# Optimization experiments

Measured on AMD Instinct MI355X. Metric: run time of the kernel, lower is better.

The kernel has to match this reference:

```python
import jax, jax.numpy as jnp
import numpy as np
from jax import lax

B, HI, WI, D = 8, 64, 64, 128
HO, WO = HI // 2, WI // 2
N_IN, N_OUT = HI * WI, HO * WO
NUM_ITERS = 3
EPS = 1e-6


def _build_indices(Ho, Wo):
    # replicates _build_q_and_in_idx: per coarse position, 9 relative offsets
    dys = np.repeat(np.arange(-1, 2), 3)
    dxs = np.tile(np.arange(-1, 2), 3)
    oy = np.arange(Ho)[:, None, None]
    ox = np.arange(Wo)[None, :, None]
    ny = oy + dys
    nx = ox + dxs
    valid = (ny >= 0) & (ny < Ho) & (nx >= 0) & (nx < Wo)  # (Ho,Wo,9)
    coarse = np.where(valid, ny * Wo + nx, 0)
    base = (oy * Wo + ox) * 9
    g9 = np.where(valid, base + np.arange(9), 0).reshape(-1, 9)
    c9 = coarse.reshape(-1, 9)
    q_idx = np.stack([np.tile(g9, (1, 4))] * 4)
    col_idx = np.stack([np.tile(c9, (1, 4))] * 4)
    in_idx = np.stack([np.tile(np.where(valid, coarse * 4 + h, 0).reshape(-1, 9), (1, 4)) for h in range(4)])
    return q_idx.astype(np.int32), in_idx.astype(np.int32), col_idx.astype(np.int32)


Q_IDX, IN_IDX, COL_IDX = _build_indices(HO, WO)
# NATTEN kernel-3 neighborhoods: window center clamped to stay in-bounds.
NY = np.clip(np.arange(HO) - 1, 0, HO - 3)[:, None] + np.arange(3)  # (HO,3)
NX = np.clip(np.arange(WO) - 1, 0, WO - 3)[:, None] + np.arange(3)  # (WO,3)


def _ln(x, g, b, eps=1e-5):
    mu = x.mean(-1, keepdims=True)
    var = ((x - mu) ** 2).mean(-1, keepdims=True)
    return (x - mu) * lax.rsqrt(var + eps) * g + b


def _forward(x, seed_w, wq, wk, wv, w1, b1, w2, b2, ln_in_g, ln_in_b, ln_out_g, ln_out_b, rpb, tau):
    ny, nx = jnp.asarray(NY), jnp.asarray(NX)
    q_idx = jnp.asarray(Q_IDX)

    def unfold(t):  # (B,HI,WI,D) -> (B,4,HO,WO,D); head = ky*2+kx (F.unfold order)
        return t.reshape(B, HO, 2, WO, 2, D).transpose(0, 2, 4, 1, 3, 5).reshape(B, 4, HO, WO, D)

    k = unfold((_ln(x, ln_in_g, ln_in_b) @ wk.T).reshape(B, HI, WI, D))
    v = unfold((x @ wv.T).reshape(B, HI, WI, D))
    k_n = k[:, :, ny][:, :, :, :, nx]  # (B,4,HO,3,WO,3,D)
    v_n = v[:, :, ny][:, :, :, :, nx]

    x_map = x.reshape(B, HI, WI, D).transpose(0, 3, 1, 2)
    seed = lax.conv_general_dilated(x_map, seed_w, (2, 2), ((1, 1), (1, 1)),
                                    dimension_numbers=('NCHW', 'OIHW', 'NCHW'))
    x_out = _ln(seed.reshape(B, D, N_OUT).transpose(0, 2, 1), ln_out_g, ln_out_b)

    scale = jnp.exp(tau)
    attn36 = a_col_h = None
    for _ in range(NUM_ITERS):
        q = (_ln(x_out, ln_out_g, ln_out_b) @ wq.T).reshape(B, HO, WO, D)
        # na2d_qk (q broadcast over the 4 heads) + relative position bias
        logits = jnp.einsum('byxd,bhykxld->bhyxkl', q, k_n).reshape(B, 4, HO, WO, 9) + rpb.reshape(1, 4, 1, 1, 9)
        attn = jax.nn.softmax(logits * scale, axis=-1) + EPS
        flat = attn.reshape(B, 4, N_OUT * 9)
        attn36 = jnp.take_along_axis(
            flat, jnp.broadcast_to(q_idx.reshape(1, 4, -1), (B, 4, N_OUT * 36)), axis=-1
        ).reshape(B, 4, N_OUT, 36)
        a_col_h = attn36 / (attn36.sum(axis=(1, 3), keepdims=True) + EPS)
        attn9 = a_col_h[..., :9].reshape(B, 4, HO, WO, 3, 3)
        # na2d_av then sum over heads
        updates = jnp.einsum('bhyxkl,bhykxld->byxd', attn9, v_n).reshape(B, N_OUT, D)
        x_out = x_out + updates
        h1 = jax.nn.gelu(x_out @ w1.T + b1, approximate=False)
        x_out = x_out + _ln(h1 @ w2.T + b2, ln_out_g, ln_out_b)
    return x_out, attn36, a_col_h


def setup_inputs() -> dict:
    key = jax.random.key(0)
    ks = jax.random.split(key, 8)
    n = lambda k, shape, s: jax.random.normal(k, shape, jnp.float32) * s
    D2 = 2 * D
    return {
        'x': jax.random.normal(ks[0], (B, N_IN, D), jnp.float32),
        'seed_w': n(ks[1], (D, D, 3, 3), (2.0 / (9 * D)) ** 0.5),
        'wq': n(ks[2], (D, D), D ** -0.5),
        'wk': n(ks[3], (D, D), D ** -0.5),
        'wv': n(ks[4], (D, D), D ** -0.5),
        'w1': n(ks[5], (D2, D), D ** -0.5),
        'b1': jnp.zeros((D2,), jnp.float32),
        'w2': n(ks[6], (D, D2), D2 ** -0.5),
        'b2': jnp.zeros((D,), jnp.float32),
        'ln_in_g': jnp.ones((D,), jnp.float32),
        'ln_in_b': jnp.zeros((D,), jnp.float32),
        'ln_out_g': jnp.ones((D,), jnp.float32),
        'ln_out_b': jnp.zeros((D,), jnp.float32),
        'rpb': n(ks[7], (4, 9), 0.02),
        'tau': jnp.float32(np.log(D ** -0.5)),
    }


def reference(x, seed_w, wq, wk, wv, w1, b1, w2, b2, ln_in_g, ln_in_b, ln_out_g, ln_out_b, rpb, tau):
    x_out, attn36, a_col_h = _forward(x, seed_w, wq, wk, wv, w1, b1, w2, b2,
                                      ln_in_g, ln_in_b, ln_out_g, ln_out_b, rpb, tau)
    # A_col: scatter_add over dim 1 -> A_col[b, in_idx[i,j], j] += a_col_h[b,i,j]
    rows = jnp.asarray(IN_IDX).reshape(4 * N_OUT, 36)
    cols = jnp.broadcast_to(jnp.arange(36), rows.shape)
    A_col = jnp.zeros((B, N_IN, N_OUT), x.dtype).at[:, rows, cols].add(a_col_h.reshape(B, 4 * N_OUT, 36))
    # A_row: scatter_add over dim 2 -> A_row[b, i, col_idx[i,j]] += attn36[b,i,j]
    ri = jnp.broadcast_to(jnp.arange(4 * N_OUT)[:, None], (4 * N_OUT, 36))
    A_row = jnp.zeros((B, N_IN, N_OUT), x.dtype).at[:, ri, jnp.asarray(COL_IDX).reshape(4 * N_OUT, 36)].add(
        attn36.reshape(B, 4 * N_OUT, 36))
    return x_out, A_row, A_col
```

## Files before the change

kernel.cpp:

```cpp
#include <hip/hip_runtime.h>
#include <hip/hip_bf16.h>
#include <math.h>

#define BB   8
#define HI_  64
#define WI_  64
#define DD   128
#define HO_  32
#define WO_  32
#define NIN  4096
#define NOUT 1024
#define LN_EPS 1e-5f
#define ATT_EPS 1e-6f

#define ZSHARE 3932160

typedef short bf16x8 __attribute__((ext_vector_type(8)));
typedef float f32x4  __attribute__((ext_vector_type(4)));

__device__ __forceinline__ ushort f2bf(float f) {
    union { float f; unsigned u; } a; a.f = f;
    unsigned u = a.u;
    return (ushort)((u + 0x7FFFu + ((u >> 16) & 1u)) >> 16);
}
__device__ __forceinline__ float bf2f(ushort u) {
    union { unsigned u; float f; } a; a.u = ((unsigned)u) << 16;
    return a.f;
}

__global__ __launch_bounds__(256)
void wconvert_kernel(const float* __restrict__ wq, const float* __restrict__ wk,
                     const float* __restrict__ wv, const float* __restrict__ w1,
                     const float* __restrict__ w2, const float* __restrict__ sw,
                     ushort* __restrict__ dst)
{
    int i = blockIdx.x * 256 + threadIdx.x;
    float v;
    if (i < 16384)        v = wk[i];
    else if (i < 32768)   v = wv[i - 16384];
    else if (i < 49152) { int j = i - 32768; int d = j >> 7, n = j & 127;
                          v = wq[n * DD + d]; }
    else if (i < 81920)   v = w1[i - 49152];
    else if (i < 114688)  v = w2[i - 81920];
    else {
        int j = i - 114688;
        int n = j / 1152;
        int rem = j - n * 1152;
        int tap = rem >> 7, di = rem & 127;
        v = sw[((size_t)(n * DD + di)) * 9 + tap];
    }
    dst[i] = f2bf(v);
}

__global__ __launch_bounds__(256)
void prep_kernel(const float* __restrict__ x, const ushort* __restrict__ wkb,
                 const ushort* __restrict__ wvb, const ushort* __restrict__ wqTb,
                 const ushort* __restrict__ wcb,
                 const float* __restrict__ ligg, const float* __restrict__ libb,
                 const float* __restrict__ logg, const float* __restrict__ lobb,
                 ushort* __restrict__ k2buf, ushort* __restrict__ vbuf,
                 float* __restrict__ xout, float4* __restrict__ zb)
{
    __shared__ __align__(16) char arena[62208];
    const int tid = threadIdx.x;
    const int wid = tid >> 6, lane = tid & 63;
    const int lr = lane & 15, lk = (lane >> 4) << 3;

    {
        float4* zp = zb + (size_t)blockIdx.x * 6144;
        float4 zz = make_float4(0.f, 0.f, 0.f, 0.f);
        #pragma unroll
        for (int i = 0; i < 24; ++i) zp[i * 256 + tid] = zz;
    }

    if (blockIdx.x < 512) {
        ushort (*Araw)[136] = (ushort (*)[136])(arena);
        ushort (*Aln)[136]  = (ushort (*)[136])(arena + 17408);
        float  (*rstat)[2]  = (float  (*)[2])(arena + 34816);
        const int row0 = blockIdx.x * 64;

        float4 xv[8];
        #pragma unroll
        for (int i = 0; i < 8; ++i) {
            int l = tid + i * 256;
            int r = l >> 5, c4 = (l & 31) << 2;
            float4 v = *(const float4*)(x + (size_t)(row0 + r) * DD + c4);
            xv[i] = v;
            ushort4 o; o.x = f2bf(v.x); o.y = f2bf(v.y); o.z = f2bf(v.z); o.w = f2bf(v.w);
            *(ushort4*)&Araw[r][c4] = o;
            float s  = v.x + v.y + v.z + v.w;
            float s2 = v.x * v.x + v.y * v.y + v.z * v.z + v.w * v.w;
            #pragma unroll
            for (int o2 = 16; o2 > 0; o2 >>= 1) {
                s  += __shfl_down(s,  o2, 32);
                s2 += __shfl_down(s2, o2, 32);
            }
            if ((tid & 31) == 0) {
                float mu = s * (1.f / DD);
                float var = s2 * (1.f / DD) - mu * mu;
                rstat[r][0] = mu; rstat[r][1] = rsqrtf(var + LN_EPS);
            }
        }
        __syncthreads();
        #pragma unroll
        for (int i = 0; i < 8; ++i) {
            int l = tid + i * 256;
            int r = l >> 5, c4 = (l & 31) << 2;
            float mu = rstat[r][0], rs = rstat[r][1];
            float4 v = xv[i];
            ushort4 o;
            o.x = f2bf((v.x - mu) * rs * ligg[c4 + 0] + libb[c4 + 0]);
            o.y = f2bf((v.y - mu) * rs * ligg[c4 + 1] + libb[c4 + 1]);
            o.z = f2bf((v.z - mu) * rs * ligg[c4 + 2] + libb[c4 + 2]);
            o.w = f2bf((v.w - mu) * rs * ligg[c4 + 3] + libb[c4 + 3]);
            *(ushort4*)&Aln[r][c4] = o;
        }
        __syncthreads();

        const int wm = (wid & 1) * 32, wn = (wid >> 1) * 64;
        {
            f32x4 ak[2][4] = {}, av[2][4] = {};
            #pragma unroll
            for (int ks = 0; ks < 4; ++ks) {
                int kk = ks * 32 + lk;
                bf16x8 aL[2], aR[2];
                #pragma unroll
                for (int mi = 0; mi < 2; ++mi) {
                    aL[mi] = *(const bf16x8*)&Aln[wm + mi * 16 + lr][kk];
                    aR[mi] = *(const bf16x8*)&Araw[wm + mi * 16 + lr][kk];
                }
                #pragma unroll
                for (int ni = 0; ni < 4; ++ni) {
                    bf16x8 bK = *(const bf16x8*)(wkb + (size_t)(wn + ni * 16 + lr) * DD + kk);
                    bf16x8 bV = *(const bf16x8*)(wvb + (size_t)(wn + ni * 16 + lr) * DD + kk);
                    #pragma unroll
                    for (int mi = 0; mi < 2; ++mi) {
                        ak[mi][ni] = __builtin_amdgcn_mfma_f32_16x16x32_bf16(aL[mi], bK, ak[mi][ni], 0, 0, 0);
                        av[mi][ni] = __builtin_amdgcn_mfma_f32_16x16x32_bf16(aR[mi], bV, av[mi][ni], 0, 0, 0);
                    }
                }
            }
            #pragma unroll
            for (int mi = 0; mi < 2; ++mi)
                #pragma unroll
                for (int ni = 0; ni < 4; ++ni) {
                    int n = wn + ni * 16 + (lane & 15);
                    #pragma unroll
                    for (int r = 0; r < 4; ++r) {
                        int m = row0 + wm + mi * 16 + ((lane >> 4) << 2) + r;
                        int b = m >> 12, pix = m & 4095;
                        int iy = pix >> 6, ix = pix & 63;
                        int h = ((iy & 1) << 1) | (ix & 1);
                        int cp = ((iy >> 1) << 5) | (ix >> 1);
                        size_t orow = ((size_t)(b * 4 + h) << 10) + cp;
                        vbuf[orow * DD + n] = f2bf(av[mi][ni][r]);
                    }
                }
            __syncthreads();
            #pragma unroll
            for (int mi = 0; mi < 2; ++mi)
                #pragma unroll
                for (int ni = 0; ni < 4; ++ni) {
                    int n = wn + ni * 16 + (lane & 15);
                    #pragma unroll
                    for (int r = 0; r < 4; ++r) {
                        int lm = wm + mi * 16 + ((lane >> 4) << 2) + r;
                        Aln[lm][n] = f2bf(ak[mi][ni][r]);
                    }
                }
        }
        __syncthreads();

        {
            f32x4 a2[2][4] = {};
            #pragma unroll
            for (int ks = 0; ks < 4; ++ks) {
                int kk = ks * 32 + lk;
                bf16x8 aF[2];
                aF[0] = *(const bf16x8*)&Aln[wm + lr][kk];
                aF[1] = *(const bf16x8*)&Aln[wm + 16 + lr][kk];
                #pragma unroll
                for (int ni = 0; ni < 4; ++ni) {
                    bf16x8 bF = *(const bf16x8*)(wqTb + (size_t)(wn + ni * 16 + lr) * DD + kk);
                    a2[0][ni] = __builtin_amdgcn_mfma_f32_16x16x32_bf16(aF[0], bF, a2[0][ni], 0, 0, 0);
                    a2[1][ni] = __builtin_amdgcn_mfma_f32_16x16x32_bf16(aF[1], bF, a2[1][ni], 0, 0, 0);
                }
            }
            #pragma unroll
            for (int mi = 0; mi < 2; ++mi)
                #pragma unroll
                for (int ni = 0; ni < 4; ++ni) {
                    int n = wn + ni * 16 + (lane & 15);
                    #pragma unroll
                    for (int r = 0; r < 4; ++r) {
                        int m = row0 + wm + mi * 16 + ((lane >> 4) << 2) + r;
                        int b = m >> 12, pix = m & 4095;
                        int iy = pix >> 6, ix = pix & 63;
                        int h = ((iy & 1) << 1) | (ix & 1);
                        int cp = ((iy >> 1) << 5) | (ix >> 1);
                        size_t orow = ((size_t)(b * 4 + h) << 10) + cp;
                        k2buf[orow * DD + n] = f2bf(a2[mi][ni][r]);
                    }
                }
        }
    } else {
        ushort (*As)[72]   = (ushort (*)[72])(arena);
        ushort (*Bs)[72]   = (ushort (*)[72])(arena + 9216);
        float  (*es)[132]  = (float  (*)[132])(arena + 27648);
        float  (*rstat)[2] = (float  (*)[2])(arena + 61440);
        const int row0 = (blockIdx.x - 512) * 64;
        const int wm = (wid & 1) * 32, wn = (wid >> 1) * 64;
        f32x4 acc[2][4] = {};

        for (int k0 = 0; k0 < 1152; k0 += 64) {
            #pragma unroll
            for (int i = 0; i < 4; ++i) {
                int l = tid + i * 256;
                int r = l >> 4, c4 = (l & 15) << 2;
                int m = row0 + r;
                int b = m >> 10, p = m & 1023;
                int y = p >> 5, xx = p & 31;
                int kg = k0 + c4;
                int tap = kg >> 7, di = kg & 127;
                int ky = tap / 3, kx = tap - ky * 3;
                int iy = 2 * y + ky - 1, ix = 2 * xx + kx - 1;
                float4 v;
                if ((unsigned)iy < (unsigned)HI_ && (unsigned)ix < (unsigned)WI_)
                    v = *(const float4*)(x + ((size_t)b * NIN + iy * WI_ + ix) * DD + di);
                else v = make_float4(0.f, 0.f, 0.f, 0.f);
                ushort4 o; o.x = f2bf(v.x); o.y = f2bf(v.y); o.z = f2bf(v.z); o.w = f2bf(v.w);
                *(ushort4*)&As[r][c4] = o;
            }
            #pragma unroll
            for (int i = 0; i < 4; ++i) {
                int l = tid + i * 256;
                int r = l >> 3, c8 = (l & 7) << 3;
                *(uint4*)&Bs[r][c8] = *(const uint4*)(wcb + (size_t)r * 1152 + k0 + c8);
            }
            __syncthreads();
            #pragma unroll
            for (int ks = 0; ks < 2; ++ks) {
                int kk = ks * 32 + lk;
                bf16x8 aF[2];
                aF[0] = *(const bf16x8*)&As[wm + lr][kk];
                aF[1] = *(const bf16x8*)&As[wm + 16 + lr][kk];
                #pragma unroll
                for (int ni = 0; ni < 4; ++ni) {
                    bf16x8 bF = *(const bf16x8*)&Bs[wn + ni * 16 + lr][kk];
                    acc[0][ni] = __builtin_amdgcn_mfma_f32_16x16x32_bf16(aF[0], bF, acc[0][ni], 0, 0, 0);
                    acc[1][ni] = __builtin_amdgcn_mfma_f32_16x16x32_bf16(aF[1], bF, acc[1][ni], 0, 0, 0);
                }
            }
            __syncthreads();
        }
        #pragma unroll
        for (int mi = 0; mi < 2; ++mi)
            #pragma unroll
            for (int ni = 0; ni < 4; ++ni) {
                int n = wn + ni * 16 + (lane & 15);
                #pragma unroll
                for (int r = 0; r < 4; ++r)
                    es[wm + mi * 16 + ((lane >> 4) << 2) + r][n] = acc[mi][ni][r];
            }
        __syncthreads();
        {
            int r = tid >> 2, q = tid & 3;
            float s = 0.f, s2 = 0.f;
            #pragma unroll
            for (int c = 0; c < 32; ++c) { float v = es[r][q * 32 + c]; s += v; s2 += v * v; }
            s += __shfl_down(s, 1, 64); s2 += __shfl_down(s2, 1, 64);
            s += __shfl_down(s, 2, 64); s2 += __shfl_down(s2, 2, 64);
            if (q == 0) {
                float mu = s * (1.f / DD);
                float var = s2 * (1.f / DD) - mu * mu;
                rstat[r][0] = mu; rstat[r][1] = rsqrtf(var + LN_EPS);
            }
        }
        __syncthreads();
        #pragma unroll
        for (int i = 0; i < 8; ++i) {
            int l = tid + i * 256;
            int r = l >> 5, c4 = (l & 31) << 2;
            float mu = rstat[r][0], rs = rstat[r][1];
            float4 o;
            o.x = (es[r][c4 + 0] - mu) * rs * logg[c4 + 0] + lobb[c4 + 0];
            o.y = (es[r][c4 + 1] - mu) * rs * logg[c4 + 1] + lobb[c4 + 1];
            o.z = (es[r][c4 + 2] - mu) * rs * logg[c4 + 2] + lobb[c4 + 2];
            o.w = (es[r][c4 + 3] - mu) * rs * logg[c4 + 3] + lobb[c4 + 3];
            *(float4*)(xout + (size_t)(row0 + r) * DD + c4) = o;
        }
    }
}

template<int LAST>
__global__ __launch_bounds__(256)
void iter_kernel(float* __restrict__ xout, const ushort* __restrict__ k2buf,
                 const ushort* __restrict__ vbuf,
                 const ushort* __restrict__ w1b, const ushort* __restrict__ w2b,
                 const float* __restrict__ b1, const float* __restrict__ b2,
                 const float* __restrict__ lg_, const float* __restrict__ lb_,
                 const float* __restrict__ rpb, const float* __restrict__ tau,
                 float* __restrict__ gbuf, float* __restrict__ denb,
                 float* __restrict__ out, float4* __restrict__ zb)
{
    const int bid = blockIdx.x;
    const int b = bid >> 6, cy = (bid >> 1) & 31, cx0 = (bid & 1) << 4;
    const int ry0 = min(max(cy - 1, 0), HO_ - 3);
    const int tid = threadIdx.x;
    const int wid = tid >> 6, lane = tid & 63;
    const int lr = lane & 15, lk = (lane >> 4) << 3;

    __shared__ float  xsf[17][132];
    __shared__ ushort qs[17][136];
    __shared__ float  rstat[17][2];
    __shared__ float  lgp[16][36];
    __shared__ float  lg0[36];
    __shared__ ushort h1s[16][264];
    __shared__ float  es[16][132];

    {
        float4* zp = zb + (size_t)blockIdx.x * 7680;
        float4 zz = make_float4(0.f, 0.f, 0.f, 0.f);
        #pragma unroll
        for (int i = 0; i < 30; ++i) zp[i * 256 + tid] = zz;
    }

    for (int l = tid; l < 544; l += 256) {
        int r = l >> 5, c4 = (l & 31) << 2;
        int g = b * NOUT + (r < 16 ? cy * 32 + cx0 + r : 0);
        *(float4*)&xsf[r][c4] = *(const float4*)(xout + (size_t)g * DD + c4);
    }
    __syncthreads();
    if (tid < 68) {
        int r = tid >> 2, q = tid & 3;
        float s = 0.f, s2 = 0.f;
        #pragma unroll
        for (int c = 0; c < 32; ++c) { float v = xsf[r][q * 32 + c]; s += v; s2 += v * v; }
        s += __shfl_down(s, 1, 64); s2 += __shfl_down(s2, 1, 64);
        s += __shfl_down(s, 2, 64); s2 += __shfl_down(s2, 2, 64);
        if (q == 0) {
            float mu = s * (1.f / DD);
            float var = s2 * (1.f / DD) - mu * mu;
            rstat[r][0] = mu; rstat[r][1] = rsqrtf(var + LN_EPS);
        }
    }
    __syncthreads();
    for (int l = tid; l < 544; l += 256) {
        int r = l >> 5, c4 = (l & 31) << 2;
        float mu = rstat[r][0], rs = rstat[r][1];
        ushort4 o;
        o.x = f2bf((xsf[r][c4 + 0] - mu) * rs * lg_[c4 + 0] + lb_[c4 + 0]);
        o.y = f2bf((xsf[r][c4 + 1] - mu) * rs * lg_[c4 + 1] + lb_[c4 + 1]);
        o.z = f2bf((xsf[r][c4 + 2] - mu) * rs * lg_[c4 + 2] + lb_[c4 + 2]);
        o.w = f2bf((xsf[r][c4 + 3] - mu) * rs * lg_[c4 + 3] + lb_[c4 + 3]);
        *(ushort4*)&qs[r][c4] = o;
    }
    __syncthreads();

    for (int task = tid; task < 612; task += 256) {
        const ushort *kp, *qp;
        int cl = 0, h, jj;
        if (task < 576) {
            cl = task / 36; int t2 = task - cl * 36;
            h = t2 / 9; jj = t2 - h * 9;
            int ky = jj / 3, kx = jj - ky * 3;
            int c = cx0 + cl;
            int nx = min(max(c - 1, 0), WO_ - 3) + kx;
            kp = k2buf + (((size_t)(b * 4 + h) << 10) + (ry0 + ky) * 32 + nx) * DD;
            qp = &qs[cl][0];
        } else {
            int t2 = task - 576;
            h = t2 / 9; jj = t2 - h * 9;
            int ky = jj / 3, kx = jj - ky * 3;
            kp = k2buf + (((size_t)(b * 4 + h) << 10) + ky * 32 + kx) * DD;
            qp = &qs[16][0];
        }
        float s = 0.f;
        #pragma unroll 4
        for (int d = 0; d < 128; d += 8) {
            uint4 ku = *(const uint4*)(kp + d);
            uint4 qu = *(const uint4*)(qp + d);
            const ushort* kk2 = (const ushort*)&ku;
            const ushort* qq2 = (const ushort*)&qu;
            #pragma unroll
            for (int t = 0; t < 8; ++t) s += bf2f(kk2[t]) * bf2f(qq2[t]);
        }
        if (task < 576) lgp[cl][h * 9 + jj] = s;
        else            lg0[task - 576] = s;
    }
    __syncthreads();

    if (tid < 64) {
        int cl = tid >> 2, h = tid & 3;
        int c = cx0 + cl;
        float scale = expf(tau[0]);
        float tmpv[9], mx = -1e30f;
        #pragma unroll
        for (int jj = 0; jj < 9; ++jj) {
            float v = (lgp[cl][h * 9 + jj] + rpb[h * 9 + jj]) * scale;
            tmpv[jj] = v; mx = fmaxf(mx, v);
        }
        float ss = 0.f;
        #pragma unroll
        for (int jj = 0; jj < 9; ++jj) { tmpv[jj] = expf(tmpv[jj] - mx); ss += tmpv[jj]; }
        float inv = 1.f / ss;
        float t0[9], mx0 = -1e30f;
        #pragma unroll
        for (int jj = 0; jj < 9; ++jj) {
            float v = (lg0[h * 9 + jj] + rpb[h * 9 + jj]) * scale;
            t0[jj] = v; mx0 = fmaxf(mx0, v);
        }
        float ss0 = 0.f;
        #pragma unroll
        for (int jj = 0; jj < 9; ++jj) ss0 += expf(t0[jj] - mx0);
        float sm0v = expf(t0[0] - mx0) / ss0 + ATT_EPS;
        float s = 0.f, gv[9];
        #pragma unroll
        for (int jj = 0; jj < 9; ++jj) {
            int dy = jj / 3 - 1, dx = jj % 3 - 1;
            bool valid = ((unsigned)(cy + dy) < (unsigned)HO_) && ((unsigned)(c + dx) < (unsigned)WO_);
            float v = valid ? (tmpv[jj] * inv + ATT_EPS) : sm0v;
            gv[jj] = v; s += v;
        }
        float tot = s;
        tot += __shfl_xor(tot, 1, 4);
        tot += __shfl_xor(tot, 2, 4);
        float dd = 4.f * tot + ATT_EPS;
        if (h == 0) denb[b * NOUT + cy * 32 + cx0 + cl] = dd;
        float invd = 1.f / dd;
        float* gp = gbuf + (((size_t)(b * 4 + h) << 10) + cy * 32 + c) * 9;
        #pragma unroll
        for (int jj = 0; jj < 9; ++jj) {
            gp[jj] = gv[jj];
            lgp[cl][h * 9 + jj] = gv[jj] * invd;
        }
    }
    __syncthreads();

    {
        int cl = tid >> 4, d0 = (tid & 15) << 3;
        int c = cx0 + cl;
        int rx0 = min(max(c - 1, 0), WO_ - 3);
        float acc8[8] = {};
        #pragma unroll
        for (int h = 0; h < 4; ++h)
            #pragma unroll
            for (int jj = 0; jj < 9; ++jj) {
                float cf = lgp[cl][h * 9 + jj];
                int ky = jj / 3, kx = jj - ky * 3;
                const ushort* vp = vbuf + (((size_t)(b * 4 + h) << 10) + (ry0 + ky) * 32 + rx0 + kx) * DD + d0;
                uint4 v0 = *(const uint4*)(vp);
                const ushort* vs0 = (const ushort*)&v0;
                #pragma unroll
                for (int t = 0; t < 8; ++t) acc8[t] += cf * bf2f(vs0[t]);
            }
        float nv[8];
        #pragma unroll
        for (int t = 0; t < 8; ++t) nv[t] = xsf[cl][d0 + t] + acc8[t];
        #pragma unroll
        for (int t = 0; t < 8; t += 4)
            *(float4*)&xsf[cl][d0 + t] = make_float4(nv[t], nv[t+1], nv[t+2], nv[t+3]);
        ushort4 q0, q1;
        q0.x = f2bf(nv[0]); q0.y = f2bf(nv[1]); q0.z = f2bf(nv[2]); q0.w = f2bf(nv[3]);
        q1.x = f2bf(nv[4]); q1.y = f2bf(nv[5]); q1.z = f2bf(nv[6]); q1.w = f2bf(nv[7]);
        *(ushort4*)&qs[cl][d0]     = q0;
        *(ushort4*)&qs[cl][d0 + 4] = q1;
    }
    __syncthreads();

    {
        const int wn = wid * 64;
        f32x4 acc[4] = {};
        #pragma unroll
        for (int ks = 0; ks < 4; ++ks) {
            int kk = ks * 32 + lk;
            bf16x8 a0 = *(const bf16x8*)&qs[lr][kk];
            #pragma unroll
            for (int ni = 0; ni < 4; ++ni) {
                bf16x8 bF = *(const bf16x8*)(w1b + (size_t)(wn + ni * 16 + lr) * DD + kk);
                acc[ni] = __builtin_amdgcn_mfma_f32_16x16x32_bf16(a0, bF, acc[ni], 0, 0, 0);
            }
        }
        #pragma unroll
        for (int ni = 0; ni < 4; ++ni) {
            int n = wn + ni * 16 + (lane & 15);
            float bv = b1[n];
            #pragma unroll
            for (int r = 0; r < 4; ++r) {
                int m = ((lane >> 4) << 2) + r;
                float v = acc[ni][r] + bv;
                v = 0.5f * v * (1.f + erff(v * 0.70710678118654752f));
                h1s[m][n] = f2bf(v);
            }
        }
    }
    __syncthreads();

    {
        const int wn = wid * 32;
        f32x4 acc[2] = {};
        #pragma unroll
        for (int ks = 0; ks < 8; ++ks) {
            int kk = ks * 32 + lk;
            bf16x8 a0 = *(const bf16x8*)&h1s[lr][kk];
            #pragma unroll
            for (int ni = 0; ni < 2; ++ni) {
                bf16x8 bF = *(const bf16x8*)(w2b + (size_t)(wn + ni * 16 + lr) * 256 + kk);
                acc[ni] = __builtin_amdgcn_mfma_f32_16x16x32_bf16(a0, bF, acc[ni], 0, 0, 0);
            }
        }
        #pragma unroll
        for (int ni = 0; ni < 2; ++ni) {
            int n = wn + ni * 16 + (lane & 15);
            float bv = b2[n];
            #pragma unroll
            for (int r = 0; r < 4; ++r)
                es[((lane >> 4) << 2) + r][n] = acc[ni][r] + bv;
        }
    }
    __syncthreads();
    if (tid < 128) {
        int r = tid >> 3, qq = tid & 7;
        float s = 0.f, s2 = 0.f;
        #pragma unroll
        for (int c = 0; c < 16; ++c) { float v = es[r][qq * 16 + c]; s += v; s2 += v * v; }
        s += __shfl_down(s, 1, 64); s2 += __shfl_down(s2, 1, 64);
        s += __shfl_down(s, 2, 64); s2 += __shfl_down(s2, 2, 64);
        s += __shfl_down(s, 4, 64); s2 += __shfl_down(s2, 4, 64);
        if (qq == 0) {
            float mu = s * (1.f / DD);
            float var = s2 * (1.f / DD) - mu * mu;
            rstat[r][0] = mu; rstat[r][1] = rsqrtf(var + LN_EPS);
        }
    }
    __syncthreads();
    for (int l = tid; l < 512; l += 256) {
        int r = l >> 5, c4 = (l & 31) << 2;
        float mu = rstat[r][0], rs = rstat[r][1];
        size_t off = ((size_t)(b * NOUT + cy * 32 + cx0 + r)) * DD + c4;
        float4 o;
        o.x = xsf[r][c4 + 0] + (es[r][c4 + 0] - mu) * rs * lg_[c4 + 0] + lb_[c4 + 0];
        o.y = xsf[r][c4 + 1] + (es[r][c4 + 1] - mu) * rs * lg_[c4 + 1] + lb_[c4 + 1];
        o.z = xsf[r][c4 + 2] + (es[r][c4 + 2] - mu) * rs * lg_[c4 + 2] + lb_[c4 + 2];
        o.w = xsf[r][c4 + 3] + (es[r][c4 + 3] - mu) * rs * lg_[c4 + 3] + lb_[c4 + 3];
        if (LAST) *(float4*)(out + off) = o;
        else      *(float4*)(xout + off) = o;
    }
}

__global__ __launch_bounds__(256)
void sparse_finish_kernel(const float* __restrict__ gbuf, const float* __restrict__ denb,
                          float* __restrict__ Arow, float* __restrict__ Acol)
{
    const int tid = threadIdx.x;
    if (blockIdx.x < 128) {
        int row = blockIdx.x * 256 + tid;
        int b = row >> 12, i = row & 4095;
        int h = i >> 10, p = i & 1023;
        int cy = p >> 5, cx = p & 31;
        const float* gp = gbuf + (((size_t)(b * 4 + h) << 10) + p) * 9;
        float* rowp = Arow + (size_t)row * NOUT;
        float acc0 = 0.f; bool has0 = false;
        #pragma unroll
        for (int jj = 0; jj < 9; ++jj) {
            int dy = jj / 3 - 1, dx = jj % 3 - 1;
            bool valid = ((unsigned)(cy + dy) < (unsigned)HO_) && ((unsigned)(cx + dx) < (unsigned)WO_);
            float g4 = 4.f * gp[jj];
            int col = (cy + dy) * WO_ + (cx + dx);
            if (valid && col != 0) rowp[col] = g4;
            else { acc0 += g4; has0 = true; }
        }
        if (has0) rowp[0] = acc0;
    } else if (blockIdx.x < 240) {
        int br = (blockIdx.x - 128) * 256 + tid;
        int b = br >> 12, r = br & 4095;
        if (r != 0) {
            int h = r & 3, coarse = r >> 2;
            int cy = coarse >> 5, cx = coarse & 31;
            float val[9];
            #pragma unroll
            for (int jj = 0; jj < 9; ++jj) {
                int dy = jj / 3 - 1, dx = jj % 3 - 1;
                int py = cy - dy, px = cx - dx;
                float v = 0.f;
                if ((unsigned)py < (unsigned)HO_ && (unsigned)px < (unsigned)WO_) {
                    int p = py * WO_ + px;
                    v = gbuf[(((size_t)(b * 4 + h) << 10) + p) * 9 + jj] / denb[b * NOUT + p];
                }
                val[jj] = v;
            }
            float* rowp = Acol + (size_t)br * NOUT;
            #pragma unroll
            for (int q = 0; q < 9; ++q) {
                float4 o = make_float4(val[(4 * q) % 9], val[(4 * q + 1) % 9],
                                       val[(4 * q + 2) % 9], val[(4 * q + 3) % 9]);
                *(float4*)(rowp + 4 * q) = o;
            }
        }
    } else if (blockIdx.x < 247) {
        const int b = blockIdx.x - 240;
        __shared__ float vals[9];
        __shared__ float wred[9][4];
        if (tid < 9) {
            int dy = tid / 3 - 1, dx = tid % 3 - 1;
            int py = -dy, px = -dx;
            float v = 0.f;
            if ((unsigned)py < (unsigned)HO_ && (unsigned)px < (unsigned)WO_) {
                int p = py * WO_ + px;
                v = gbuf[(((size_t)(b * 4 + 0) << 10) + p) * 9 + tid] / denb[b * NOUT + p];
            }
            vals[tid] = v;
        }
        float part[9] = {};
        for (int p = tid; p < NOUT; p += 256) {
            float invd = 1.f / denb[b * NOUT + p];
            int py = p >> 5, px = p & 31;
            #pragma unroll
            for (int jj = 0; jj < 9; ++jj) {
                int dy = jj / 3 - 1, dx = jj % 3 - 1;
                bool valid = ((unsigned)(py + dy) < (unsigned)HO_) && ((unsigned)(px + dx) < (unsigned)WO_);
                if (!valid) part[jj] += invd;
            }
        }
        #pragma unroll
        for (int jj = 0; jj < 9; ++jj) {
            float s = part[jj];
            #pragma unroll
            for (int o = 32; o > 0; o >>= 1) s += __shfl_down(s, o, 64);
            if ((tid & 63) == 0) wred[jj][tid >> 6] = s;
        }
        __syncthreads();
        if (tid < 9) {
            float s = wred[tid][0] + wred[tid][1] + wred[tid][2] + wred[tid][3];
            float H = 0.f;
            for (int h2 = 0; h2 < 4; ++h2)
                H += gbuf[(((size_t)(b * 4 + h2)) << 10) * 9];
            vals[tid] += H * s;
        }
        __syncthreads();
        if (tid < 36) Acol[(size_t)(b * 4096) * NOUT + tid] = vals[tid % 9];
    } else {
        const int br = 28672 + (blockIdx.x - 247);
        const int b = br >> 12, r = br & 4095;
        const int h = r & 3, coarse = r >> 2;
        const int cy = coarse >> 5, cx = coarse & 31;
        __shared__ float vals[9];
        __shared__ float wred[9][4];
        if (tid < 9) {
            int dy = tid / 3 - 1, dx = tid % 3 - 1;
            int py = cy - dy, px = cx - dx;
            float v = 0.f;
            if ((unsigned)py < (unsigned)HO_ && (unsigned)px < (unsigned)WO_) {
                int p = py * WO_ + px;
                v = gbuf[(((size_t)(b * 4 + h) << 10) + p) * 9 + tid] / denb[b * NOUT + p];
            }
            vals[tid] = v;
        }
        if (r == 0) {
            float part[9] = {};
            for (int p = tid; p < NOUT; p += 256) {
                float invd = 1.f / denb[b * NOUT + p];
                int py = p >> 5, px = p & 31;
                #pragma unroll
                for (int jj = 0; jj < 9; ++jj) {
                    int dy = jj / 3 - 1, dx = jj % 3 - 1;
                    bool valid = ((unsigned)(py + dy) < (unsigned)HO_) && ((unsigned)(px + dx) < (unsigned)WO_);
                    if (!valid) part[jj] += invd;
                }
            }
            #pragma unroll
            for (int jj = 0; jj < 9; ++jj) {
                float s = part[jj];
                #pragma unroll
                for (int o = 32; o > 0; o >>= 1) s += __shfl_down(s, o, 64);
                if ((tid & 63) == 0) wred[jj][tid >> 6] = s;
            }
            __syncthreads();
            if (tid < 9) {
                float s = wred[tid][0] + wred[tid][1] + wred[tid][2] + wred[tid][3];
                float H = 0.f;
                for (int h2 = 0; h2 < 4; ++h2)
                    H += gbuf[(((size_t)(b * 4 + h2)) << 10) * 9];
                vals[tid] += H * s;
            }
        }
        __syncthreads();
        float* rowp = Acol + (size_t)br * NOUT;
        int c4 = tid << 2;
        float o[4];
        #pragma unroll
        for (int e = 0; e < 4; ++e) {
            int c = c4 + e;
            o[e] = (c < 36) ? vals[c % 9] : 0.f;
        }
        *(float4*)(rowp + c4) = make_float4(o[0], o[1], o[2], o[3]);
    }
}

extern "C" void kernel_launch(void* const* d_in, const int* in_sizes, int n_in,
                              void* d_out, int out_size, void* d_ws, size_t ws_size,
                              hipStream_t stream)
{
    const float* x        = (const float*)d_in[0];
    const float* seed_w   = (const float*)d_in[1];
    const float* wq       = (const float*)d_in[2];
    const float* wk       = (const float*)d_in[3];
    const float* wv       = (const float*)d_in[4];
    const float* w1       = (const float*)d_in[5];
    const float* b1       = (const float*)d_in[6];
    const float* w2       = (const float*)d_in[7];
    const float* b2       = (const float*)d_in[8];
    const float* ln_in_g  = (const float*)d_in[9];
    const float* ln_in_b  = (const float*)d_in[10];
    const float* ln_out_g = (const float*)d_in[11];
    const float* ln_out_b = (const float*)d_in[12];
    const float* rpb      = (const float*)d_in[13];
    const float* tau      = (const float*)d_in[14];

    float* out  = (float*)d_out;
    float* Arow = out + (size_t)BB * NOUT * DD;
    float* Acol = Arow + (size_t)BB * NIN * NOUT;
    float4* zb  = (float4*)Arow;

    float* ws    = (float*)d_ws;
    float* xout  = ws;
    float* gbuf  = xout + (size_t)BB * NOUT * DD;
    float* denb  = gbuf + (size_t)BB * 4 * NOUT * 9;
    ushort* wb   = (ushort*)(denb + BB * NOUT);
    ushort* wkb  = wb;
    ushort* wvb  = wb + 16384;
    ushort* wqTb = wb + 32768;
    ushort* w1b  = wb + 49152;
    ushort* w2b  = wb + 81920;
    ushort* wcb  = wb + 114688;

    ushort* k2buf = (ushort*)(Acol + (size_t)28672 * NOUT);
    ushort* vbuf  = k2buf + (size_t)4194304;

    wconvert_kernel<<<1024, 256, 0, stream>>>(wq, wk, wv, w1, w2, seed_w, wb);
    prep_kernel<<<640, 256, 0, stream>>>(x, wkb, wvb, wqTb, wcb, ln_in_g, ln_in_b,
                                         ln_out_g, ln_out_b, k2buf, vbuf, xout,
                                         zb + (size_t)0 * ZSHARE);

    iter_kernel<0><<<BB * HO_ * 2, 256, 0, stream>>>(
        xout, k2buf, vbuf, w1b, w2b, b1, b2, ln_out_g, ln_out_b,
        rpb, tau, gbuf, denb, out, zb + (size_t)1 * ZSHARE);
    iter_kernel<0><<<BB * HO_ * 2, 256, 0, stream>>>(
        xout, k2buf, vbuf, w1b, w2b, b1, b2, ln_out_g, ln_out_b,
        rpb, tau, gbuf, denb, out, zb + (size_t)2 * ZSHARE);
    iter_kernel<1><<<BB * HO_ * 2, 256, 0, stream>>>(
        xout, k2buf, vbuf, w1b, w2b, b1, b2, ln_out_g, ln_out_b,
        rpb, tau, gbuf, denb, out, zb + (size_t)3 * ZSHARE);

    sparse_finish_kernel<<<4343, 256, 0, stream>>>(gbuf, denb, Arow, Acol);
}
```

Baseline: 179.5 us.

## Split seed-conv into 16-row tiles and fuse LN stats into iter epilogue

The seed convolution branch of prep_kernel now handles 16 output rows per block instead of 64, which raises the grid from 640 to 1024 blocks, shrinks the shared-memory arena, and rebalances the zero-fill chunk per block. The aim is more parallelism and occupancy for the conv GEMM, at the cost of reloading weight tiles from global memory more often. In iter_kernel, the output LayerNorm statistics are now reduced with wave shuffles straight from the MFMA accumulators into a small partial-sum array. This removes a shared-memory pass and a barrier-separated reduction stage.

```diff
diff --git a/kernel.cpp b/kernel.cpp
--- a/kernel.cpp
+++ b/kernel.cpp
@@ -61,16 +61,16 @@
                  ushort* __restrict__ k2buf, ushort* __restrict__ vbuf,
                  float* __restrict__ xout, float4* __restrict__ zb)
 {
-    __shared__ __align__(16) char arena[62208];
+    __shared__ __align__(16) char arena[35328];
     const int tid = threadIdx.x;
     const int wid = tid >> 6, lane = tid & 63;
     const int lr = lane & 15, lk = (lane >> 4) << 3;
 
     {
-        float4* zp = zb + (size_t)blockIdx.x * 6144;
+        float4* zp = zb + (size_t)blockIdx.x * 3840;
         float4 zz = make_float4(0.f, 0.f, 0.f, 0.f);
         #pragma unroll
-        for (int i = 0; i < 24; ++i) zp[i * 256 + tid] = zz;
+        for (int i = 0; i < 15; ++i) zp[i * 256 + tid] = zz;
     }
 
     if (blockIdx.x < 512) {
@@ -205,18 +205,16 @@
         }
     } else {
         ushort (*As)[72]   = (ushort (*)[72])(arena);
-        ushort (*Bs)[72]   = (ushort (*)[72])(arena + 9216);
-        float  (*es)[132]  = (float  (*)[132])(arena + 27648);
-        float  (*rstat)[2] = (float  (*)[2])(arena + 61440);
-        const int row0 = (blockIdx.x - 512) * 64;
-        const int wm = (wid & 1) * 32, wn = (wid >> 1) * 64;
-        f32x4 acc[2][4] = {};
+        ushort (*Bs)[72]   = (ushort (*)[72])(arena + 2304);
+        float  (*es)[132]  = (float  (*)[132])(arena + 20736);
+        float  (*rstat)[2] = (float  (*)[2])(arena + 29184);
+        const int row0 = (blockIdx.x - 512) * 16;
+        const int wn = wid * 32;
+        f32x4 acc[2] = {};
 
         for (int k0 = 0; k0 < 1152; k0 += 64) {
-            #pragma unroll
-            for (int i = 0; i < 4; ++i) {
-                int l = tid + i * 256;
-                int r = l >> 4, c4 = (l & 15) << 2;
+            {
+                int r = tid >> 4, c4 = (tid & 15) << 2;
                 int m = row0 + r;
                 int b = m >> 10, p = m & 1023;
                 int y = p >> 5, xx = p & 31;
@@ -241,29 +239,24 @@
             #pragma unroll
             for (int ks = 0; ks < 2; ++ks) {
                 int kk = ks * 32 + lk;
-                bf16x8 aF[2];
-                aF[0] = *(const bf16x8*)&As[wm + lr][kk];
-                aF[1] = *(const bf16x8*)&As[wm + 16 + lr][kk];
-                #pragma unroll
-                for (int ni = 0; ni < 4; ++ni) {
+                bf16x8 a0 = *(const bf16x8*)&As[lr][kk];
+                #pragma unroll
+                for (int ni = 0; ni < 2; ++ni) {
                     bf16x8 bF = *(const bf16x8*)&Bs[wn + ni * 16 + lr][kk];
-                    acc[0][ni] = __builtin_amdgcn_mfma_f32_16x16x32_bf16(aF[0], bF, acc[0][ni], 0, 0, 0);
-                    acc[1][ni] = __builtin_amdgcn_mfma_f32_16x16x32_bf16(aF[1], bF, acc[1][ni], 0, 0, 0);
+                    acc[ni] = __builtin_amdgcn_mfma_f32_16x16x32_bf16(a0, bF, acc[ni], 0, 0, 0);
                 }
             }
             __syncthreads();
         }
         #pragma unroll
-        for (int mi = 0; mi < 2; ++mi)
-            #pragma unroll
-            for (int ni = 0; ni < 4; ++ni) {
-                int n = wn + ni * 16 + (lane & 15);
-                #pragma unroll
-                for (int r = 0; r < 4; ++r)
-                    es[wm + mi * 16 + ((lane >> 4) << 2) + r][n] = acc[mi][ni][r];
-            }
+        for (int ni = 0; ni < 2; ++ni) {
+            int n = wn + ni * 16 + (lane & 15);
+            #pragma unroll
+            for (int r = 0; r < 4; ++r)
+                es[((lane >> 4) << 2) + r][n] = acc[ni][r];
+        }
         __syncthreads();
-        {
+        if (tid < 64) {
             int r = tid >> 2, q = tid & 3;
             float s = 0.f, s2 = 0.f;
             #pragma unroll
@@ -278,7 +271,7 @@
         }
         __syncthreads();
         #pragma unroll
-        for (int i = 0; i < 8; ++i) {
+        for (int i = 0; i < 2; ++i) {
             int l = tid + i * 256;
             int r = l >> 5, c4 = (l & 31) << 2;
             float mu = rstat[r][0], rs = rstat[r][1];
@@ -317,6 +310,7 @@
     __shared__ float  lg0[36];
     __shared__ ushort h1s[16][264];
     __shared__ float  es[16][132];
+    __shared__ float  fp2[16][4][2];
 
     {
         float4* zp = zb + (size_t)blockIdx.x * 7680;
@@ -509,34 +503,31 @@
                 acc[ni] = __builtin_amdgcn_mfma_f32_16x16x32_bf16(a0, bF, acc[ni], 0, 0, 0);
             }
         }
-        #pragma unroll
-        for (int ni = 0; ni < 2; ++ni) {
-            int n = wn + ni * 16 + (lane & 15);
-            float bv = b2[n];
-            #pragma unroll
-            for (int r = 0; r < 4; ++r)
-                es[((lane >> 4) << 2) + r][n] = acc[ni][r] + bv;
-        }
-    }
-    __syncthreads();
-    if (tid < 128) {
-        int r = tid >> 3, qq = tid & 7;
-        float s = 0.f, s2 = 0.f;
-        #pragma unroll
-        for (int c = 0; c < 16; ++c) { float v = es[r][qq * 16 + c]; s += v; s2 += v * v; }
-        s += __shfl_down(s, 1, 64); s2 += __shfl_down(s2, 1, 64);
-        s += __shfl_down(s, 2, 64); s2 += __shfl_down(s2, 2, 64);
-        s += __shfl_down(s, 4, 64); s2 += __shfl_down(s2, 4, 64);
-        if (qq == 0) {
-            float mu = s * (1.f / DD);
-            float var = s2 * (1.f / DD) - mu * mu;
-            rstat[r][0] = mu; rstat[r][1] = rsqrtf(var + LN_EPS);
+        float bv0 = b2[wn + (lane & 15)];
+        float bv1 = b2[wn + 16 + (lane & 15)];
+        #pragma unroll
+        for (int r = 0; r < 4; ++r) {
+            int m = ((lane >> 4) << 2) + r;
+            float v0 = acc[0][r] + bv0;
+            float v1 = acc[1][r] + bv1;
+            es[m][wn + (lane & 15)] = v0;
+            es[m][wn + 16 + (lane & 15)] = v1;
+            float s = v0 + v1, s2 = v0 * v0 + v1 * v1;
+            #pragma unroll
+            for (int o = 1; o < 16; o <<= 1) {
+                s  += __shfl_down(s,  o, 16);
+                s2 += __shfl_down(s2, o, 16);
+            }
+            if ((lane & 15) == 0) { fp2[m][wid][0] = s; fp2[m][wid][1] = s2; }
         }
     }
     __syncthreads();
     for (int l = tid; l < 512; l += 256) {
         int r = l >> 5, c4 = (l & 31) << 2;
-        float mu = rstat[r][0], rs = rstat[r][1];
+        float s  = fp2[r][0][0] + fp2[r][1][0] + fp2[r][2][0] + fp2[r][3][0];
+        float s2 = fp2[r][0][1] + fp2[r][1][1] + fp2[r][2][1] + fp2[r][3][1];
+        float mu = s * (1.f / DD);
+        float rs = rsqrtf(s2 * (1.f / DD) - mu * mu + LN_EPS);
         size_t off = ((size_t)(b * NOUT + cy * 32 + cx0 + r)) * DD + c4;
         float4 o;
         o.x = xsf[r][c4 + 0] + (es[r][c4 + 0] - mu) * rs * lg_[c4 + 0] + lb_[c4 + 0];
@@ -738,9 +729,9 @@
     ushort* vbuf  = k2buf + (size_t)4194304;
 
     wconvert_kernel<<<1024, 256, 0, stream>>>(wq, wk, wv, w1, w2, seed_w, wb);
-    prep_kernel<<<640, 256, 0, stream>>>(x, wkb, wvb, wqTb, wcb, ln_in_g, ln_in_b,
-                                         ln_out_g, ln_out_b, k2buf, vbuf, xout,
-                                         zb + (size_t)0 * ZSHARE);
+    prep_kernel<<<1024, 256, 0, stream>>>(x, wkb, wvb, wqTb, wcb, ln_in_g, ln_in_b,
+                                          ln_out_g, ln_out_b, k2buf, vbuf, xout,
+                                          zb + (size_t)0 * ZSHARE);
 
     iter_kernel<0><<<BB * HO_ * 2, 256, 0, stream>>>(
         xout, k2buf, vbuf, w1b, w2b, b1, b2, ln_out_g, ln_out_b,
```

Result: faster. 164.9 us (-8.1%).
